# Kernel optimization log

Hardware: AMD Instinct MI355X
Metric: run time of the kernel (lower is better)

Reference implementation:

```python
import jax, jax.numpy as jnp
import numpy as np

B, SQ, SK, D = 8, 4096, 4096, 128


def setup_inputs() -> dict:
    key = jax.random.key(0)
    kq, kk, kv = jax.random.split(key, 3)
    return {
        "q1": jax.random.normal(kq, (B, SQ, D), dtype=jnp.float32),
        "k1": jax.random.normal(kk, (B, SK, D), dtype=jnp.float32),
        "v1": jax.random.normal(kv, (B, SK, D), dtype=jnp.float32),
        "inv_scale_factor": jnp.float32(np.sqrt(D)),  # QK is divided by this
        "dropout_p": jnp.float32(0.1),
        "dropout_m": jnp.float32(0.1),
        "dropout_inplace": 1,  # no-op in functional JAX
    }


def reference(q1, k1, v1, inv_scale_factor, dropout_p, dropout_m, dropout_inplace):
    # qk = q1 @ k1^T ; scaled = qk / inv_scale_factor ; softmax over keys
    qk = jnp.einsum("bqd,bkd->bqk", q1, k1)
    softmax_qk = jax.nn.softmax(qk / inv_scale_factor, axis=-1)
    # torch: mask = F.dropout(ones_like(sm), p) -> bernoulli(1-p)/(1-p)
    keep = jax.random.bernoulli(jax.random.key(42), 1.0 - dropout_p, softmax_qk.shape)
    mask = keep.astype(softmax_qk.dtype) / (1.0 - dropout_p)
    # non-standard: divide by (1 - dropout_m) instead of (1 - dropout_p)
    dropout_qk = softmax_qk * mask / (1.0 - dropout_m)
    return jnp.einsum("bqk,bkd->bqd", dropout_qk, v1)
```

## Files before the change

kernel.cpp:

```cpp
#include <hip/hip_runtime.h>
#include <stdint.h>

#define Bn  8
#define SQn 4096
#define SKn 4096
#define Dn  128
#define QTn 64
#define KTn 64
static constexpr uint32_t NTOT = 134217728u;

typedef __attribute__((ext_vector_type(8))) short short8;
typedef __attribute__((ext_vector_type(4))) short short4v;
typedef __attribute__((ext_vector_type(4))) float f32x4;

__device__ __forceinline__ short f2bf(float f) {
  uint32_t x = __float_as_uint(f);
  uint32_t r = (x + 0x7FFFu + ((x >> 16) & 1u)) >> 16;
  return (short)r;
}

__device__ __forceinline__ uint32_t rotl32(uint32_t x, uint32_t r) {
  return (x << r) | (x >> (32u - r));
}

__device__ __forceinline__ void tf2x32(uint32_t x0, uint32_t x1, uint32_t& o0, uint32_t& o1) {
  const uint32_t k0 = 0u, k1 = 42u, k2 = 0x1BD11BF0u;
  x0 += k0; x1 += k1;
#define TFR(r) { x0 += x1; x1 = rotl32(x1, r); x1 ^= x0; }
  TFR(13) TFR(15) TFR(26) TFR(6)  x0 += k1; x1 += k2 + 1u;
  TFR(17) TFR(29) TFR(16) TFR(24) x0 += k2; x1 += k0 + 2u;
  TFR(13) TFR(15) TFR(26) TFR(6)  x0 += k0; x1 += k1 + 3u;
  TFR(17) TFR(29) TFR(16) TFR(24) x0 += k1; x1 += k2 + 4u;
  TFR(13) TFR(15) TFR(26) TFR(6)  x0 += k2; x1 += k0 + 5u;
#undef TFR
  o0 = x0; o1 = x1;
}

__device__ __forceinline__ bool keep_from_bits(uint32_t bits, float pkeep) {
  float u = __uint_as_float((bits >> 9) | 0x3F800000u) - 1.0f;
  return u < pkeep;
}

template <int N>
__device__ __forceinline__ float ror16(float x) {
  int xi = __float_as_int(x);
  int r = __builtin_amdgcn_update_dpp(xi, xi, 0x120 | N, 0xF, 0xF, false);
  return __int_as_float(r);
}
__device__ __forceinline__ float redmax16(float x) {
  x = fmaxf(x, ror16<8>(x)); x = fmaxf(x, ror16<4>(x));
  x = fmaxf(x, ror16<2>(x)); x = fmaxf(x, ror16<1>(x));
  return x;
}
__device__ __forceinline__ float redsum16(float x) {
  x += ror16<8>(x); x += ror16<4>(x); x += ror16<2>(x); x += ror16<1>(x);
  return x;
}

__global__ __launch_bounds__(256) void mask_gen(const float* __restrict__ p_pd,
                                                uint32_t* __restrict__ mask) {
  uint32_t T = blockIdx.x * 256u + threadIdx.x;
  float pkeep = 1.0f - p_pd[0];
  uint32_t base = T * 32u;
  uint32_t w0 = 0u;
#pragma unroll 8
  for (uint32_t j = 0; j < 32u; j++) {
    uint32_t o0, o1;
    tf2x32(0u, base + j, o0, o1);
    w0 |= (keep_from_bits(o0 ^ o1, pkeep) ? 1u : 0u) << j;
  }
  mask[T] = w0;
}

template <int USE_MASK>
__global__ __launch_bounds__(256, 2) void attn(
    const float* __restrict__ Qg, const float* __restrict__ Kg, const float* __restrict__ Vg,
    const float* __restrict__ p_inv, const float* __restrict__ p_pd, const float* __restrict__ p_pm,
    const uint2* __restrict__ maskw2, float* __restrict__ Out) {
  __shared__ __align__(16) short Kt[KTn * Dn];
  __shared__ __align__(16) short Vt[Dn * KTn];
  __shared__ __align__(16) short Pt[QTn * 72];

  const int tid = threadIdx.x;
  const int w = tid >> 6;
  const int lane = tid & 63;
  const int m = lane & 15;
  const int h = lane >> 4;
  const int gid = blockIdx.x;
  const int b = gid & 7;
  const int q0 = (gid >> 3) * QTn;

  const float rscale = 1.0f / p_inv[0];
  const float pd = p_pd[0], pm = p_pm[0];
  const float pkeep = 1.0f - pd;
  const float oscale_c = 1.0f / ((1.0f - pd) * (1.0f - pm));

  short8 qf[4];
  {
    const float* qp = Qg + ((size_t)(b * SQn + q0 + w * 16 + m)) * Dn;
#pragma unroll
    for (int c = 0; c < 4; c++) {
      float4 a = *reinterpret_cast<const float4*>(qp + c * 32 + h * 8);
      float4 a2 = *reinterpret_cast<const float4*>(qp + c * 32 + h * 8 + 4);
      short8 v;
      v[0] = f2bf(a.x * rscale);  v[1] = f2bf(a.y * rscale);
      v[2] = f2bf(a.z * rscale);  v[3] = f2bf(a.w * rscale);
      v[4] = f2bf(a2.x * rscale); v[5] = f2bf(a2.y * rscale);
      v[6] = f2bf(a2.z * rscale); v[7] = f2bf(a2.w * rscale);
      qf[c] = v;
    }
  }

  f32x4 acc[8];
#pragma unroll
  for (int dt = 0; dt < 8; dt++) acc[dt] = (f32x4){0.f, 0.f, 0.f, 0.f};
  float m_run[4], l_run[4];
  uint32_t rowb[4];
#pragma unroll
  for (int r = 0; r < 4; r++) {
    m_run[r] = -1e30f;
    l_run[r] = 0.f;
    rowb[r] = (uint32_t)(b * SQn + q0 + w * 16 + 4 * h + r) * (uint32_t)SKn;
  }

  const size_t kvbase = (size_t)b * SKn * Dn;

  float4 kreg[8], vreg[8];
  auto issue_loads = [&](int kt) {
    const float* kp = Kg + kvbase + (size_t)kt * KTn * Dn;
    const float* vp = Vg + kvbase + (size_t)kt * KTn * Dn;
#pragma unroll
    for (int p = 0; p < 8; p++) {
      int idx = p * 256 + tid;
      kreg[p] = *reinterpret_cast<const float4*>(kp + (idx >> 5) * Dn + (idx & 31) * 4);
    }
#pragma unroll
    for (int p = 0; p < 4; p++) {
      int idx = p * 256 + tid;
      int kp2 = idx >> 5, dq = idx & 31;
      vreg[2 * p]     = *reinterpret_cast<const float4*>(vp + (2 * kp2) * Dn + dq * 4);
      vreg[2 * p + 1] = *reinterpret_cast<const float4*>(vp + (2 * kp2 + 1) * Dn + dq * 4);
    }
  };
  auto write_tiles = [&]() {
#pragma unroll
    for (int p = 0; p < 8; p++) {
      int idx = p * 256 + tid;
      int row = idx >> 5, dq = idx & 31;
      float4 x = kreg[p];
      short4v sv;
      sv[0] = f2bf(x.x); sv[1] = f2bf(x.y); sv[2] = f2bf(x.z); sv[3] = f2bf(x.w);
      *reinterpret_cast<short4v*>(&Kt[row * 128 + ((dq * 4) ^ ((row & 7) << 3))]) = sv;
    }
#pragma unroll
    for (int p = 0; p < 4; p++) {
      int idx = p * 256 + tid;
      int kp2 = idx >> 5, dq = idx & 31;
      int swz = (dq & 7) << 3;
      float4 v0 = vreg[2 * p], v1 = vreg[2 * p + 1];
      const float* f0 = &v0.x;
      const float* f1 = &v1.x;
#pragma unroll
      for (int i = 0; i < 4; i++) {
        int d = dq * 4 + i;
        uint32_t pk = ((uint32_t)(uint16_t)f2bf(f0[i])) |
                      (((uint32_t)(uint16_t)f2bf(f1[i])) << 16);
        *reinterpret_cast<uint32_t*>(&Vt[d * 64 + ((2 * kp2) ^ swz)]) = pk;
      }
    }
  };
  auto load_mask = [&](int kt, uint2* dst) {
#pragma unroll
    for (int r = 0; r < 4; r++) {
      uint32_t widx = (uint32_t)(b * SQn + q0 + w * 16 + 4 * h + r) * 64u + (uint32_t)kt;
      dst[r] = maskw2[widx];
    }
  };

  issue_loads(0);
  uint2 mw_nxt[4];
  if (USE_MASK) load_mask(0, mw_nxt);

  for (int kt = 0; kt < SKn / KTn; kt++) {
    __syncthreads();
    write_tiles();
    if (kt + 1 < SKn / KTn) issue_loads(kt + 1);
    uint2 mw[4];
    if (USE_MASK) {
#pragma unroll
      for (int r = 0; r < 4; r++) mw[r] = mw_nxt[r];
      if (kt + 1 < SKn / KTn) load_mask(kt + 1, mw_nxt);
    }
    __syncthreads();

    f32x4 sfr[4];
#pragma unroll
    for (int t = 0; t < 4; t++) {
      f32x4 s = (f32x4){0.f, 0.f, 0.f, 0.f};
      int krow = t * 16 + m;
      int swzk = (krow & 7) << 3;
#pragma unroll
      for (int c = 0; c < 4; c++) {
        short8 kf = *reinterpret_cast<const short8*>(
            &Kt[krow * 128 + ((c * 32 + h * 8) ^ swzk)]);
        s = __builtin_amdgcn_mfma_f32_16x16x32_bf16(qf[c], kf, s, 0, 0, 0);
      }
      sfr[t] = s;
    }

    float oscl[4];
    float pv[4][4];
#pragma unroll
    for (int r = 0; r < 4; r++) {
      float s0 = sfr[0][r], s1 = sfr[1][r], s2 = sfr[2][r], s3 = sfr[3][r];
      float tmax = redmax16(fmaxf(fmaxf(s0, s1), fmaxf(s2, s3)));
      float mnew = fmaxf(m_run[r], tmax);
      float al = __expf(m_run[r] - mnew);
      float e0 = __expf(s0 - mnew), e1 = __expf(s1 - mnew);
      float e2 = __expf(s2 - mnew), e3 = __expf(s3 - mnew);
      float ts = redsum16(e0 + e1 + e2 + e3);
      l_run[r] = l_run[r] * al + ts;
      m_run[r] = mnew;
      oscl[r] = al;
      pv[0][r] = e0; pv[1][r] = e1; pv[2][r] = e2; pv[3][r] = e3;
    }
#pragma unroll
    for (int dt = 0; dt < 8; dt++) {
#pragma unroll
      for (int r = 0; r < 4; r++) acc[dt][r] *= oscl[r];
    }

#pragma unroll
    for (int r = 0; r < 4; r++) {
      int qrow = w * 16 + 4 * h + r;
      int psw = (qrow & 8) << 1;
#pragma unroll
      for (int t = 0; t < 4; t++) {
        bool kp;
        if (USE_MASK) {
          uint32_t wm = (t < 2) ? mw[r].x : mw[r].y;
          kp = (wm >> ((t & 1) * 16 + m)) & 1u;
        } else {
          uint32_t n = rowb[r] + (uint32_t)(kt * 64 + t * 16 + m);
          uint32_t o0, o1;
          tf2x32(0u, n, o0, o1);
          kp = keep_from_bits(o0 ^ o1, pkeep);
        }
        float pmv = kp ? pv[t][r] : 0.0f;
        Pt[qrow * 72 + ((t * 16 + m) ^ psw)] = f2bf(pmv);
      }
    }

    {
      int qr = w * 16 + m;
      int psw = (qr & 8) << 1;
#pragma unroll
      for (int c = 0; c < 2; c++) {
        short8 pa = *reinterpret_cast<const short8*>(&Pt[qr * 72 + ((c * 32 + h * 8) ^ psw)]);
#pragma unroll
        for (int dt = 0; dt < 8; dt++) {
          int d = dt * 16 + m;
          short8 vb = *reinterpret_cast<const short8*>(
              &Vt[d * 64 + ((c * 32 + h * 8) ^ (((d >> 2) & 7) << 3))]);
          acc[dt] = __builtin_amdgcn_mfma_f32_16x16x32_bf16(pa, vb, acc[dt], 0, 0, 0);
        }
      }
    }
  }

#pragma unroll
  for (int r = 0; r < 4; r++) {
    float os = oscale_c / l_run[r];
    float* op = Out + (size_t)(b * SQn + q0 + w * 16 + 4 * h + r) * Dn;
#pragma unroll
    for (int dt = 0; dt < 8; dt++) op[dt * 16 + m] = acc[dt][r] * os;
  }
}

extern "C" void kernel_launch(void* const* d_in, const int* in_sizes, int n_in,
                              void* d_out, int out_size, void* d_ws, size_t ws_size,
                              hipStream_t stream) {
  const float* Qg = (const float*)d_in[0];
  const float* Kg = (const float*)d_in[1];
  const float* Vg = (const float*)d_in[2];
  const float* p_inv = (const float*)d_in[3];
  const float* p_pd = (const float*)d_in[4];
  const float* p_pm = (const float*)d_in[5];
  float* Out = (float*)d_out;

  const bool use_mask = ws_size >= (size_t)(NTOT / 8u);
  if (use_mask) {
    mask_gen<<<dim3(NTOT / 32u / 256u), dim3(256), 0, stream>>>(p_pd, (uint32_t*)d_ws);
    attn<1><<<dim3(512), dim3(256), 0, stream>>>(Qg, Kg, Vg, p_inv, p_pd, p_pm,
                                                 (const uint2*)d_ws, Out);
  } else {
    attn<0><<<dim3(512), dim3(256), 0, stream>>>(Qg, Kg, Vg, p_inv, p_pd, p_pm,
                                                 nullptr, Out);
  }
}
```

Measured before the change: 558.4 us.

## Generate dropout mask inline in attention kernel instead of separate mask pass

Drops the separate mask-generation kernel and its 16 MB workspace bitmask, which the attention kernel used to read back. The Threefry bits are now computed inline in the attention inner loop for every score element. The Threefry rotate uses alignbit and the keep test is an integer threshold compare instead of a float conversion. This removes the mask write/read traffic and one launch, but adds about 20 rounds of integer ALU work per element to the attention kernel, which may compete with the MFMA and softmax work.

After: 496.3 us. 11.1% less time.

```diff
diff --git a/kernel.cpp b/kernel.cpp
--- a/kernel.cpp
+++ b/kernel.cpp
@@ -7,7 +7,6 @@
 #define Dn  128
 #define QTn 64
 #define KTn 64
-static constexpr uint32_t NTOT = 134217728u;
 
 typedef __attribute__((ext_vector_type(8))) short short8;
 typedef __attribute__((ext_vector_type(4))) short short4v;
@@ -19,11 +18,11 @@
   return (short)r;
 }
 
-__device__ __forceinline__ uint32_t rotl32(uint32_t x, uint32_t r) {
-  return (x << r) | (x >> (32u - r));
-}
-
-__device__ __forceinline__ void tf2x32(uint32_t x0, uint32_t x1, uint32_t& o0, uint32_t& o1) {
+__device__ __forceinline__ uint32_t rotl32(uint32_t x, int r) {
+  return __builtin_amdgcn_alignbit(x, x, (32 - r) & 31);
+}
+
+__device__ __forceinline__ uint32_t tf2x32_xor(uint32_t x0, uint32_t x1) {
   const uint32_t k0 = 0u, k1 = 42u, k2 = 0x1BD11BF0u;
   x0 += k0; x1 += k1;
 #define TFR(r) { x0 += x1; x1 = rotl32(x1, r); x1 ^= x0; }
@@ -33,12 +32,7 @@
   TFR(17) TFR(29) TFR(16) TFR(24) x0 += k1; x1 += k2 + 4u;
   TFR(13) TFR(15) TFR(26) TFR(6)  x0 += k2; x1 += k0 + 5u;
 #undef TFR
-  o0 = x0; o1 = x1;
-}
-
-__device__ __forceinline__ bool keep_from_bits(uint32_t bits, float pkeep) {
-  float u = __uint_as_float((bits >> 9) | 0x3F800000u) - 1.0f;
-  return u < pkeep;
+  return x0 ^ x1;
 }
 
 template <int N>
@@ -57,26 +51,10 @@
   return x;
 }
 
-__global__ __launch_bounds__(256) void mask_gen(const float* __restrict__ p_pd,
-                                                uint32_t* __restrict__ mask) {
-  uint32_t T = blockIdx.x * 256u + threadIdx.x;
-  float pkeep = 1.0f - p_pd[0];
-  uint32_t base = T * 32u;
-  uint32_t w0 = 0u;
-#pragma unroll 8
-  for (uint32_t j = 0; j < 32u; j++) {
-    uint32_t o0, o1;
-    tf2x32(0u, base + j, o0, o1);
-    w0 |= (keep_from_bits(o0 ^ o1, pkeep) ? 1u : 0u) << j;
-  }
-  mask[T] = w0;
-}
-
-template <int USE_MASK>
 __global__ __launch_bounds__(256, 2) void attn(
     const float* __restrict__ Qg, const float* __restrict__ Kg, const float* __restrict__ Vg,
     const float* __restrict__ p_inv, const float* __restrict__ p_pd, const float* __restrict__ p_pm,
-    const uint2* __restrict__ maskw2, float* __restrict__ Out) {
+    float* __restrict__ Out) {
   __shared__ __align__(16) short Kt[KTn * Dn];
   __shared__ __align__(16) short Vt[Dn * KTn];
   __shared__ __align__(16) short Pt[QTn * 72];
@@ -92,7 +70,7 @@
 
   const float rscale = 1.0f / p_inv[0];
   const float pd = p_pd[0], pm = p_pm[0];
-  const float pkeep = 1.0f - pd;
+  const uint32_t ithr = (uint32_t)ceilf((1.0f - pd) * 8388608.0f);
   const float oscale_c = 1.0f / ((1.0f - pd) * (1.0f - pm));
 
   short8 qf[4];
@@ -169,28 +147,13 @@
       }
     }
   };
-  auto load_mask = [&](int kt, uint2* dst) {
-#pragma unroll
-    for (int r = 0; r < 4; r++) {
-      uint32_t widx = (uint32_t)(b * SQn + q0 + w * 16 + 4 * h + r) * 64u + (uint32_t)kt;
-      dst[r] = maskw2[widx];
-    }
-  };
 
   issue_loads(0);
-  uint2 mw_nxt[4];
-  if (USE_MASK) load_mask(0, mw_nxt);
 
   for (int kt = 0; kt < SKn / KTn; kt++) {
     __syncthreads();
     write_tiles();
     if (kt + 1 < SKn / KTn) issue_loads(kt + 1);
-    uint2 mw[4];
-    if (USE_MASK) {
-#pragma unroll
-      for (int r = 0; r < 4; r++) mw[r] = mw_nxt[r];
-      if (kt + 1 < SKn / KTn) load_mask(kt + 1, mw_nxt);
-    }
     __syncthreads();
 
     f32x4 sfr[4];
@@ -230,22 +193,16 @@
       for (int r = 0; r < 4; r++) acc[dt][r] *= oscl[r];
     }
 
+    const uint32_t kbase = (uint32_t)(kt * 64 + m);
 #pragma unroll
     for (int r = 0; r < 4; r++) {
       int qrow = w * 16 + 4 * h + r;
       int psw = (qrow & 8) << 1;
+      uint32_t nb = rowb[r] + kbase;
 #pragma unroll
       for (int t = 0; t < 4; t++) {
-        bool kp;
-        if (USE_MASK) {
-          uint32_t wm = (t < 2) ? mw[r].x : mw[r].y;
-          kp = (wm >> ((t & 1) * 16 + m)) & 1u;
-        } else {
-          uint32_t n = rowb[r] + (uint32_t)(kt * 64 + t * 16 + m);
-          uint32_t o0, o1;
-          tf2x32(0u, n, o0, o1);
-          kp = keep_from_bits(o0 ^ o1, pkeep);
-        }
+        uint32_t bits = tf2x32_xor(0u, nb + (uint32_t)(t * 16));
+        bool kp = (bits >> 9) < ithr;
         float pmv = kp ? pv[t][r] : 0.0f;
         Pt[qrow * 72 + ((t * 16 + m) ^ psw)] = f2bf(pmv);
       }
@@ -288,13 +245,5 @@
   const float* p_pm = (const float*)d_in[5];
   float* Out = (float*)d_out;
 
-  const bool use_mask = ws_size >= (size_t)(NTOT / 8u);
-  if (use_mask) {
-    mask_gen<<<dim3(NTOT / 32u / 256u), dim3(256), 0, stream>>>(p_pd, (uint32_t*)d_ws);
-    attn<1><<<dim3(512), dim3(256), 0, stream>>>(Qg, Kg, Vg, p_inv, p_pd, p_pm,
-                                                 (const uint2*)d_ws, Out);
-  } else {
-    attn<0><<<dim3(512), dim3(256), 0, stream>>>(Qg, Kg, Vg, p_inv, p_pd, p_pm,
-                                                 nullptr, Out);
-  }
-}
+  attn<<<dim3(512), dim3(256), 0, stream>>>(Qg, Kg, Vg, p_inv, p_pd, p_pm, Out);
+}
```
